# Performance work log

Hardware: AMD Instinct MI355X
Metric: run time of the kernel (lower is better)

The kernel has to match this reference:

```python
import jax, jax.numpy as jnp
import numpy as np

N_NODES = 50000
N_EDGES = 800000
N_GRAPHS = 2048
NODE_F = 30
EDGE_F = 8
HID = 32
HEADS = 4
NEG_SLOPE = 0.2


def _gat_conv(x, src, dst, eattr, W, a_src, a_dst, We, a_edge, b):
    # x: [N, Fin]; src/dst: [E'] (self-loops already appended); eattr: [E', edge_dim]
    N = x.shape[0]
    H, C = a_src.shape
    h = (x @ W).reshape(N, H, C)                     # [N,H,C]
    e = (eattr @ We).reshape(-1, H, C)               # [E',H,C]
    al_s = jnp.sum(h * a_src, axis=-1)               # [N,H]
    al_d = jnp.sum(h * a_dst, axis=-1)               # [N,H]
    al_e = jnp.sum(e * a_edge, axis=-1)              # [E',H]
    alpha = al_s[src] + al_d[dst] + al_e             # [E',H]
    alpha = jax.nn.leaky_relu(alpha, NEG_SLOPE)
    # segment softmax over destination nodes (every node has a self-loop)
    mx = jax.ops.segment_max(alpha, dst, num_segments=N)
    alpha = jnp.exp(alpha - mx[dst])
    den = jax.ops.segment_sum(alpha, dst, num_segments=N)
    alpha = alpha / (den[dst] + 1e-16)
    msg = h[src] * alpha[:, :, None]                 # [E',H,C]
    out = jax.ops.segment_sum(msg, dst, num_segments=N)  # [N,H,C]
    return out.reshape(N, H * C) + b


def _make_params(key):
    ks = jax.random.split(key, 32)
    i = 0
    p = {}
    def nxt(shape, scale=0.1):
        nonlocal i
        k = ks[i]; i += 1
        return jax.random.normal(k, shape, dtype=jnp.float32) * scale
    dims = [(NODE_F, HEADS * HID), (HEADS * HID, HEADS * HID), (HEADS * HID, HEADS * HID)]
    for li, (fin, fout) in enumerate(dims, 1):
        p[f"W{li}"] = nxt((fin, fout))
        p[f"att_src{li}"] = nxt((HEADS, HID))
        p[f"att_dst{li}"] = nxt((HEADS, HID))
        p[f"We{li}"] = nxt((EDGE_F, HEADS * HID))
        p[f"att_e{li}"] = nxt((HEADS, HID))
        p[f"b{li}"] = nxt((HEADS * HID,))
    p["lw1"] = nxt((HEADS * HID, HID)); p["lb1"] = nxt((HID,))
    p["lw2"] = nxt((HID, HID)); p["lb2"] = nxt((HID,))
    p["lw3"] = nxt((HID, 1)); p["lb3"] = nxt((1,))
    return p


def setup_inputs() -> dict:
    key = jax.random.key(0)
    k1, k2, k3, k4, k5 = jax.random.split(key, 5)
    x = jax.random.normal(k1, (N_NODES, NODE_F), dtype=jnp.float32)
    edge_index = jax.random.randint(k2, (2, N_EDGES), 0, N_NODES, dtype=jnp.int64)
    edge_features = jax.random.normal(k3, (N_EDGES, EDGE_F), dtype=jnp.float32)
    batch = jnp.sort(jax.random.randint(k4, (N_NODES,), 0, N_GRAPHS, dtype=jnp.int64))
    inp = {"x": x, "edge_index": edge_index, "edge_features": edge_features, "batch": batch}
    inp.update(_make_params(k5))
    return inp


def reference(x, edge_index, edge_features, batch,
              W1, att_src1, att_dst1, We1, att_e1, b1,
              W2, att_src2, att_dst2, We2, att_e2, b2,
              W3, att_src3, att_dst3, We3, att_e3, b3,
              lw1, lb1, lw2, lb2, lw3, lb3):
    N = x.shape[0]
    # add self-loops (PyG GATConv default); self-loop edge_attr = mean of edge_attr
    loop = jnp.arange(N, dtype=edge_index.dtype)
    src = jnp.concatenate([edge_index[0], loop])
    dst = jnp.concatenate([edge_index[1], loop])
    mean_e = jnp.mean(edge_features, axis=0, keepdims=True)
    eattr = jnp.concatenate([edge_features, jnp.broadcast_to(mean_e, (N, EDGE_F))], axis=0)

    h = jax.nn.relu(_gat_conv(x, src, dst, eattr, W1, att_src1, att_dst1, We1, att_e1, b1))
    h = jax.nn.relu(_gat_conv(h, src, dst, eattr, W2, att_src2, att_dst2, We2, att_e2, b2))
    h = jax.nn.relu(_gat_conv(h, src, dst, eattr, W3, att_src3, att_dst3, We3, att_e3, b3))
    # global_add_pool
    g = jax.ops.segment_sum(h, batch, num_segments=N_GRAPHS)   # [G, H*C]
    g = jax.nn.relu(g @ lw1 + lb1)
    g = jax.nn.relu(g @ lw2 + lb2)
    g = jax.nn.relu(g @ lw3 + lb3)                              # [G, 1]
    return g
```

## Files before the change

kernel.cpp:

```cpp
#include <hip/hip_runtime.h>

#define NND 50000
#define NE  800000
#define NET 850000
#define NG  2048
#define KT  32
#define SCB 196
#define MB  1024

__device__ __forceinline__ float frelu(float v){ return v > 0.f ? v : 0.f; }

__device__ __forceinline__ unsigned short f2bf(float f){
    unsigned int u = __float_as_uint(f);
    u += 0x7FFFu + ((u >> 16) & 1u);
    return (unsigned short)(u >> 16);
}

__global__ __launch_bounds__(256) void k_mean(const float4* __restrict__ ef4,
                                              float* __restrict__ partial){
    __shared__ float4 red[256];
    int t = threadIdx.x;
    int i0 = blockIdx.x * 256 + t;
    const int S = MB * 256;
    float4 a = make_float4(0.f, 0.f, 0.f, 0.f);
    for (int j = i0; j < NE * 2; j += S){
        float4 v = ef4[j];
        a.x += v.x; a.y += v.y; a.z += v.z; a.w += v.w;
    }
    red[t] = a;
    __syncthreads();
    for (int off = 128; off >= 2; off >>= 1){
        if (t < off){
            float4 o = red[t + off];
            float4 m = red[t];
            m.x += o.x; m.y += o.y; m.z += o.z; m.w += o.w;
            red[t] = m;
        }
        __syncthreads();
    }
    if (t < 8){
        float v = (t < 4) ? ((const float*)&red[0])[t]
                          : ((const float*)&red[1])[t - 4];
        partial[blockIdx.x * 8 + t] = v;
    }
}

__global__ void k_prep(const float* __restrict__ partial,
                       const float* __restrict__ We1, const float* __restrict__ ae1,
                       const float* __restrict__ We2, const float* __restrict__ ae2,
                       const float* __restrict__ We3, const float* __restrict__ ae3,
                       float* __restrict__ M, float* __restrict__ sc){
    __shared__ float me[8];
    __shared__ float pm[16][8];
    __shared__ float Ms[96];
    int t = threadIdx.x;
    {
        int ch = t & 7, seg = t >> 3;
        float s = 0.f;
        for (int j = seg; j < MB; j += 16) s += partial[j * 8 + ch];
        pm[seg][ch] = s;
    }
    __syncthreads();
    if (t < 8){
        float s = 0.f;
        for (int i = 0; i < 16; i++) s += pm[i][t];
        me[t] = s * (1.0f / NE);
    }
    if (t < 96){
        int l = t >> 5, f = (t >> 2) & 7, h = t & 3;
        const float* We = (l == 0) ? We1 : ((l == 1) ? We2 : We3);
        const float* ae = (l == 0) ? ae1 : ((l == 1) ? ae2 : ae3);
        float s = 0.f;
        for (int c = 0; c < 32; c++) s += We[f * 128 + h * 32 + c] * ae[h * 32 + c];
        M[t] = s; Ms[t] = s;
    }
    __syncthreads();
    if (t < 12){
        int l = t >> 2, h = t & 3;
        float s = 0.f;
        for (int f = 0; f < 8; f++) s += me[f] * Ms[l * 32 + f * 4 + h];
        sc[t] = s;
    }
}

__global__ __launch_bounds__(256) void k_gemm(
        const float* __restrict__ x, const float* __restrict__ W,
        const float* __restrict__ asrc, const float* __restrict__ adst,
        unsigned short* __restrict__ h, float* __restrict__ als,
        float* __restrict__ ald, int Fin){
    __shared__ float Ws[KT * 128];
    __shared__ float xst[KT * 36];
    int t  = threadIdx.x;
    int cg = t & 31;
    int rg = t >> 5;
    int r0 = blockIdx.x * 32;
    float acc[4][4] = {{0.f}};
    int nch = (Fin + KT - 1) / KT;
    for (int ch = 0; ch < nch; ch++){
        int k0 = ch * KT;
        {
            const float4* Wv = (const float4*)(W + k0 * 128);
            float4* Wsv = (float4*)Ws;
            int lim = (Fin - k0 >= KT ? KT : Fin - k0) * 32;
            for (int i = t; i < KT * 32; i += 256)
                Wsv[i] = (i < lim) ? Wv[i] : make_float4(0.f, 0.f, 0.f, 0.f);
        }
        for (int i = t; i < 32 * KT; i += 256){
            int r = i >> 5, kk = i & 31;
            int gr = r0 + r;
            float v = 0.f;
            if (gr < NND && (k0 + kk) < Fin) v = x[gr * Fin + k0 + kk];
            xst[kk * 36 + r] = v;
        }
        __syncthreads();
        #pragma unroll 8
        for (int k = 0; k < KT; k++){
            float4 xv = *(const float4*)&xst[k * 36 + rg * 4];
            float4 wv = *(const float4*)&Ws[k * 128 + cg * 4];
            acc[0][0] += xv.x * wv.x; acc[0][1] += xv.x * wv.y;
            acc[0][2] += xv.x * wv.z; acc[0][3] += xv.x * wv.w;
            acc[1][0] += xv.y * wv.x; acc[1][1] += xv.y * wv.y;
            acc[1][2] += xv.y * wv.z; acc[1][3] += xv.y * wv.w;
            acc[2][0] += xv.z * wv.x; acc[2][1] += xv.z * wv.y;
            acc[2][2] += xv.z * wv.z; acc[2][3] += xv.z * wv.w;
            acc[3][0] += xv.w * wv.x; acc[3][1] += xv.w * wv.y;
            acc[3][2] += xv.w * wv.z; acc[3][3] += xv.w * wv.w;
        }
        __syncthreads();
    }
    float4 av = *(const float4*)&asrc[cg * 4];
    float4 dv = *(const float4*)&adst[cg * 4];
    int head = cg >> 3;
    bool leader = ((cg & 7) == 0);
    #pragma unroll
    for (int r = 0; r < 4; r++){
        int gr = r0 + rg * 4 + r;
        float4 o = make_float4(acc[r][0], acc[r][1], acc[r][2], acc[r][3]);
        if (gr < NND){
            ushort4 p;
            p.x = f2bf(o.x); p.y = f2bf(o.y); p.z = f2bf(o.z); p.w = f2bf(o.w);
            *(ushort4*)&h[gr * 128 + cg * 4] = p;
        }
        float sv = o.x * av.x + o.y * av.y + o.z * av.z + o.w * av.w;
        float sd = o.x * dv.x + o.y * dv.y + o.z * dv.z + o.w * dv.w;
        sv += __shfl_down(sv, 4, 64); sd += __shfl_down(sd, 4, 64);
        sv += __shfl_down(sv, 2, 64); sd += __shfl_down(sd, 2, 64);
        sv += __shfl_down(sv, 1, 64); sd += __shfl_down(sd, 1, 64);
        if (leader && gr < NND){
            als[gr * 4 + head] = sv;
            ald[gr * 4 + head] = sd;
        }
    }
}

__global__ void k_hist(const int* __restrict__ ei, int* __restrict__ cnt,
                       int* __restrict__ pose){
    int e = blockIdx.x * 256 + threadIdx.x;
    if (e >= NE) return;
    int d = ei[NE + e];
    pose[e] = atomicAdd(&cnt[d], 1);
}

__global__ __launch_bounds__(256) void k_scan1(const int* __restrict__ cnt,
                                               int* __restrict__ bsum){
    __shared__ int red[256];
    int t = threadIdx.x;
    int idx = blockIdx.x * 256 + t;
    red[t] = (idx < NND) ? (cnt[idx] + 1) : 0;
    __syncthreads();
    for (int off = 128; off > 0; off >>= 1){
        if (t < off) red[t] += red[t + off];
        __syncthreads();
    }
    if (t == 0) bsum[blockIdx.x] = red[0];
}

__global__ __launch_bounds__(256) void k_scan2(const int* __restrict__ bsum,
                                               int* __restrict__ boff,
                                               int* __restrict__ rs){
    __shared__ int ls[256];
    int t = threadIdx.x;
    int v = (t < SCB) ? bsum[t] : 0;
    ls[t] = v;
    __syncthreads();
    for (int off = 1; off < 256; off <<= 1){
        int u = (t >= off) ? ls[t - off] : 0;
        __syncthreads();
        ls[t] += u;
        __syncthreads();
    }
    if (t < SCB) boff[t] = ls[t] - bsum[t];
    if (t == 0)  rs[NND] = ls[255];
}

__global__ __launch_bounds__(256) void k_scan3(const int* __restrict__ cnt,
                                               const int* __restrict__ boff,
                                               int* __restrict__ rs){
    __shared__ int ls[256];
    int t = threadIdx.x;
    int idx = blockIdx.x * 256 + t;
    int v = (idx < NND) ? (cnt[idx] + 1) : 0;
    ls[t] = v;
    __syncthreads();
    for (int off = 1; off < 256; off <<= 1){
        int u = (t >= off) ? ls[t - off] : 0;
        __syncthreads();
        ls[t] += u;
        __syncthreads();
    }
    if (idx < NND) rs[idx] = boff[blockIdx.x] + ls[t] - v;
}

__global__ void k_scatter(const int* __restrict__ ei, const int* __restrict__ rs,
                          const int* __restrict__ pose, int* __restrict__ srcarr,
                          int* __restrict__ slotof){
    int e = blockIdx.x * 256 + threadIdx.x;
    if (e >= NET) return;
    if (e < NE){
        int s = ei[e], d = ei[NE + e];
        int slot = rs[d] + 1 + pose[e];
        srcarr[slot] = s;
        slotof[e] = slot;
    } else {
        int n = e - NE;
        srcarr[rs[n]] = n;
    }
}

__global__ __launch_bounds__(256) void k_weight(
        const int* __restrict__ ei, const float* __restrict__ ef,
        const float4* __restrict__ als4, const float4* __restrict__ ald4,
        const float* __restrict__ Mg, const float* __restrict__ sc4g,
        const int* __restrict__ rs, const int* __restrict__ slotof,
        float4* __restrict__ wS){
    __shared__ float Ms[32];
    __shared__ float Scs[4];
    int t = threadIdx.x;
    if (t < 32) Ms[t] = Mg[t];
    if (t < 4)  Scs[t] = sc4g[t];
    __syncthreads();
    int e = blockIdx.x * 256 + t;
    if (e < NE){
        int s = ei[e], d = ei[NE + e];
        const float4* efp = (const float4*)ef;
        float4 u = efp[e * 2], v = efp[e * 2 + 1];
        float4 A = als4[s], D = ald4[d];
        float4 w;
        float* wp = &w.x;
        const float* Ap = &A.x; const float* Dp = &D.x;
        #pragma unroll
        for (int h = 0; h < 4; h++){
            float ae = u.x * Ms[0 + h]  + u.y * Ms[4 + h]
                     + u.z * Ms[8 + h]  + u.w * Ms[12 + h]
                     + v.x * Ms[16 + h] + v.y * Ms[20 + h]
                     + v.z * Ms[24 + h] + v.w * Ms[28 + h];
            float a = Ap[h] + Dp[h] + ae;
            a = a > 0.f ? a : 0.2f * a;
            wp[h] = __expf(a);
        }
        wS[slotof[e]] = w;
    } else if (e < NE + NND){
        int n = e - NE;
        float4 A = als4[n], D = ald4[n];
        float4 w;
        float* wp = &w.x;
        const float* Ap = &A.x; const float* Dp = &D.x;
        #pragma unroll
        for (int h = 0; h < 4; h++){
            float a = Ap[h] + Dp[h] + Scs[h];
            a = a > 0.f ? a : 0.2f * a;
            wp[h] = __expf(a);
        }
        wS[rs[n]] = w;
    }
}

__global__ __launch_bounds__(256) void k_gather(
        const int* __restrict__ srcarr, const int* __restrict__ rs,
        const float* __restrict__ wS,
        const unsigned int* __restrict__ HU,
        const float* __restrict__ b, float* __restrict__ out){
    int wid  = threadIdx.x >> 6;
    int lane = threadIdx.x & 63;
    int n = blockIdx.x * 4 + wid;
    int start = rs[n], end = rs[n + 1];
    int cnt = end - start;
    int mh = lane >> 4;
    float ax = 0.f, ay = 0.f, accw = 0.f;

    int s[8]; float w[8];
    int k = 0;
    if (cnt >= 8){
        #pragma unroll
        for (int j = 0; j < 8; j++){
            int i = start + j;
            s[j] = srcarr[i];
            w[j] = wS[i * 4 + mh];
        }
    }
    while (k + 8 <= cnt){
        int cs[8]; float cw[8];
        #pragma unroll
        for (int j = 0; j < 8; j++){ cs[j] = s[j]; cw[j] = w[j]; }
        k += 8;
        if (k + 8 <= cnt){
            #pragma unroll
            for (int j = 0; j < 8; j++){
                int i = start + k + j;
                s[j] = srcarr[i];
                w[j] = wS[i * 4 + mh];
            }
        }
        unsigned int hv[8];
        #pragma unroll
        for (int j = 0; j < 8; j++) hv[j] = HU[cs[j] * 64 + lane];
        #pragma unroll
        for (int j = 0; j < 8; j++){
            float lo = __uint_as_float(hv[j] << 16);
            float hi = __uint_as_float(hv[j] & 0xFFFF0000u);
            ax += cw[j] * lo;
            ay += cw[j] * hi;
            accw += cw[j];
        }
    }
    int rem = cnt - k;
    if (rem > 0){
        int ts[8]; float tw[8];
        #pragma unroll
        for (int j = 0; j < 8; j++){
            bool v = j < rem;
            int i = v ? (start + k + j) : start;
            ts[j] = srcarr[i];
            tw[j] = v ? wS[i * 4 + mh] : 0.f;
        }
        unsigned int hv[8];
        #pragma unroll
        for (int j = 0; j < 8; j++) hv[j] = HU[ts[j] * 64 + lane];
        #pragma unroll
        for (int j = 0; j < 8; j++){
            float lo = __uint_as_float(hv[j] << 16);
            float hi = __uint_as_float(hv[j] & 0xFFFF0000u);
            ax += tw[j] * lo;
            ay += tw[j] * hi;
            accw += tw[j];
        }
    }
    float inv = 1.f / (accw + 1e-16f);
    int c0 = 2 * lane;
    float2 o;
    o.x = frelu(ax * inv + b[c0]);
    o.y = frelu(ay * inv + b[c0 + 1]);
    ((float2*)out)[n * 64 + lane] = o;
}

__global__ __launch_bounds__(128) void k_pool(const float* __restrict__ y,
                                              const int* __restrict__ batch,
                                              float* __restrict__ g){
    int c = threadIdx.x;
    int n0 = blockIdx.x * 32;
    if (n0 >= NND) return;
    int cur = batch[n0];
    float s = 0.f;
    for (int k = 0; k < 32; k++){
        int n = n0 + k;
        if (n >= NND) break;
        int bg = batch[n];
        if (bg != cur){
            atomicAdd(&g[cur * 128 + c], s);
            s = 0.f; cur = bg;
        }
        s += y[n * 128 + c];
    }
    atomicAdd(&g[cur * 128 + c], s);
}

__global__ void k_mlp(const float* __restrict__ g,
                      const float* __restrict__ lw1, const float* __restrict__ lb1,
                      const float* __restrict__ lw2, const float* __restrict__ lb2,
                      const float* __restrict__ lw3, const float* __restrict__ lb3,
                      float* __restrict__ out){
    __shared__ float t1[4][32];
    __shared__ float t2[4][32];
    int tid = threadIdx.x, sub = tid >> 5, j = tid & 31;
    int gi = blockIdx.x * 4 + sub;
    const float* gr = g + gi * 128;
    float s = lb1[j];
    for (int c = 0; c < 128; c++) s += gr[c] * lw1[c * 32 + j];
    t1[sub][j] = frelu(s);
    __syncthreads();
    float s2 = lb2[j];
    for (int k = 0; k < 32; k++) s2 += t1[sub][k] * lw2[k * 32 + j];
    t2[sub][j] = frelu(s2);
    __syncthreads();
    if (j == 0){
        float o = lb3[0];
        for (int k = 0; k < 32; k++) o += t2[sub][k] * lw3[k];
        out[gi] = frelu(o);
    }
}

extern "C" void kernel_launch(void* const* d_in, const int* in_sizes, int n_in,
                              void* d_out, int out_size, void* d_ws, size_t ws_size,
                              hipStream_t stream) {
    const float* x     = (const float*)d_in[0];
    const int*   ei    = (const int*)  d_in[1];
    const float* ef    = (const float*)d_in[2];
    const int*   batch = (const int*)  d_in[3];
    const float* W[3]   = {(const float*)d_in[4],  (const float*)d_in[10], (const float*)d_in[16]};
    const float* as_[3] = {(const float*)d_in[5],  (const float*)d_in[11], (const float*)d_in[17]};
    const float* ad_[3] = {(const float*)d_in[6],  (const float*)d_in[12], (const float*)d_in[18]};
    const float* We[3]  = {(const float*)d_in[7],  (const float*)d_in[13], (const float*)d_in[19]};
    const float* ae[3]  = {(const float*)d_in[8],  (const float*)d_in[14], (const float*)d_in[20]};
    const float* b_[3]  = {(const float*)d_in[9],  (const float*)d_in[15], (const float*)d_in[21]};
    const float* lw1 = (const float*)d_in[22]; const float* lb1 = (const float*)d_in[23];
    const float* lw2 = (const float*)d_in[24]; const float* lb2 = (const float*)d_in[25];
    const float* lw3 = (const float*)d_in[26]; const float* lb3 = (const float*)d_in[27];

    float* ws = (float*)d_ws;
    float* Bx   = ws;
    float* Hbf  = Bx + 6400000;
    float* wSf  = Hbf + 6400000;
    float* als  = wSf + 3400000;
    float* ald  = als + 200000;
    float* g    = ald + 200000;
    float* partial = g + 262144;
    float* M    = partial + MB * 8;
    float* sc   = M + 96;
    int*   srcarr = (int*)(sc + 16);
    int*   slotof = srcarr + NET;
    int*   pose   = slotof + NE;
    int*   rs     = pose + NE;
    int*   cnt    = rs + NND + 4;
    int*   bsum   = cnt + NND;
    int*   boff   = bsum + SCB;

    unsigned short* Hb = (unsigned short*)Hbf;

    hipMemsetAsync(cnt, 0, NND * sizeof(int), stream);
    hipMemsetAsync(g,   0, NG * 128 * sizeof(float), stream);

    k_mean<<<MB, 256, 0, stream>>>((const float4*)ef, partial);
    k_prep<<<1, 128, 0, stream>>>(partial, We[0], ae[0], We[1], ae[1], We[2], ae[2], M, sc);

    k_hist<<<(NE + 255) / 256, 256, 0, stream>>>(ei, cnt, pose);
    k_scan1<<<SCB, 256, 0, stream>>>(cnt, bsum);
    k_scan2<<<1, 256, 0, stream>>>(bsum, boff, rs);
    k_scan3<<<SCB, 256, 0, stream>>>(cnt, boff, rs);
    k_scatter<<<(NET + 255) / 256, 256, 0, stream>>>(ei, rs, pose, srcarr, slotof);

    const float* xin = x;
    for (int l = 0; l < 3; l++){
        int Fin = (l == 0) ? 30 : 128;
        k_gemm<<<(NND + 31) / 32, 256, 0, stream>>>(xin, W[l], as_[l], ad_[l],
                                                    Hb, als, ald, Fin);
        k_weight<<<(NE + NND + 255) / 256, 256, 0, stream>>>(
            ei, ef, (const float4*)als, (const float4*)ald,
            M + l * 32, sc + l * 4, rs, slotof, (float4*)wSf);
        k_gather<<<NND / 4, 256, 0, stream>>>(srcarr, rs, wSf,
                                              (const unsigned int*)Hb, b_[l], Bx);
        xin = Bx;
    }

    k_pool<<<(NND + 31) / 32, 128, 0, stream>>>(Bx, batch, g);
    k_mlp<<<NG / 4, 128, 0, stream>>>(g, lw1, lb1, lw2, lb2, lw3, lb3, (float*)d_out);
}
```

Before: 475.2 us.

## Rewrite node GEMM with bf16 MFMA and LDS-staged epilogue

Replaces the FP32 scalar register-tiled node-feature GEMM with a bf16 MFMA (16x16x32) kernel that processes 64 rows per block. The input is converted to bf16 in LDS, and the per-head attention dot products are computed from the bf16 results staged in LDS. Output rows are then written with coalesced 16-byte stores. The feature width is made a template parameter. Inputs are now rounded to bf16 before the multiply, which lowers precision, and attention logits are computed from rounded h instead of the fp32 accumulators.

Measured after the change: 472.6 us. No clear change (-0.5%).

```diff
diff --git a/kernel.cpp b/kernel.cpp
--- a/kernel.cpp
+++ b/kernel.cpp
@@ -4,9 +4,11 @@
 #define NE  800000
 #define NET 850000
 #define NG  2048
-#define KT  32
 #define SCB 196
 #define MB  1024
+
+typedef __attribute__((ext_vector_type(8))) short short8;
+typedef __attribute__((ext_vector_type(4))) float float4v;
 
 __device__ __forceinline__ float frelu(float v){ return v > 0.f ? v : 0.f; }
 
@@ -83,73 +85,87 @@
     }
 }
 
+template<int FIN, int FINR>
 __global__ __launch_bounds__(256) void k_gemm(
         const float* __restrict__ x, const float* __restrict__ W,
         const float* __restrict__ asrc, const float* __restrict__ adst,
         unsigned short* __restrict__ h, float* __restrict__ als,
-        float* __restrict__ ald, int Fin){
-    __shared__ float Ws[KT * 128];
-    __shared__ float xst[KT * 36];
-    int t  = threadIdx.x;
-    int cg = t & 31;
-    int rg = t >> 5;
-    int r0 = blockIdx.x * 32;
-    float acc[4][4] = {{0.f}};
-    int nch = (Fin + KT - 1) / KT;
-    for (int ch = 0; ch < nch; ch++){
-        int k0 = ch * KT;
-        {
-            const float4* Wv = (const float4*)(W + k0 * 128);
-            float4* Wsv = (float4*)Ws;
-            int lim = (Fin - k0 >= KT ? KT : Fin - k0) * 32;
-            for (int i = t; i < KT * 32; i += 256)
-                Wsv[i] = (i < lim) ? Wv[i] : make_float4(0.f, 0.f, 0.f, 0.f);
-        }
-        for (int i = t; i < 32 * KT; i += 256){
-            int r = i >> 5, kk = i & 31;
-            int gr = r0 + r;
-            float v = 0.f;
-            if (gr < NND && (k0 + kk) < Fin) v = x[gr * Fin + k0 + kk];
-            xst[kk * 36 + r] = v;
-        }
-        __syncthreads();
-        #pragma unroll 8
-        for (int k = 0; k < KT; k++){
-            float4 xv = *(const float4*)&xst[k * 36 + rg * 4];
-            float4 wv = *(const float4*)&Ws[k * 128 + cg * 4];
-            acc[0][0] += xv.x * wv.x; acc[0][1] += xv.x * wv.y;
-            acc[0][2] += xv.x * wv.z; acc[0][3] += xv.x * wv.w;
-            acc[1][0] += xv.y * wv.x; acc[1][1] += xv.y * wv.y;
-            acc[1][2] += xv.y * wv.z; acc[1][3] += xv.y * wv.w;
-            acc[2][0] += xv.z * wv.x; acc[2][1] += xv.z * wv.y;
-            acc[2][2] += xv.z * wv.z; acc[2][3] += xv.z * wv.w;
-            acc[3][0] += xv.w * wv.x; acc[3][1] += xv.w * wv.y;
-            acc[3][2] += xv.w * wv.z; acc[3][3] += xv.w * wv.w;
-        }
-        __syncthreads();
-    }
-    float4 av = *(const float4*)&asrc[cg * 4];
-    float4 dv = *(const float4*)&adst[cg * 4];
-    int head = cg >> 3;
-    bool leader = ((cg & 7) == 0);
+        float* __restrict__ ald){
+    constexpr int KS = FIN + 8;
+    constexpr int SZ1 = 64 * KS + 128 * KS;
+    constexpr int SZ2 = 64 * 136;
+    constexpr int LSZ = SZ1 > SZ2 ? SZ1 : SZ2;
+    __shared__ unsigned short lds[LSZ];
+    unsigned short* xa = lds;
+    unsigned short* wb = lds + 64 * KS;
+    int t = threadIdx.x;
+    int r0 = blockIdx.x * 64;
+
+    for (int i = t; i < 64 * (FIN / 2); i += 256){
+        int r = i / (FIN / 2), kp = i % (FIN / 2);
+        int gr = r0 + r, k = 2 * kp;
+        float v0 = 0.f, v1 = 0.f;
+        if (gr < NND){
+            if (k     < FINR) v0 = x[gr * FINR + k];
+            if (k + 1 < FINR) v1 = x[gr * FINR + k + 1];
+        }
+        unsigned int pk = (unsigned int)f2bf(v0) | ((unsigned int)f2bf(v1) << 16);
+        *(unsigned int*)&xa[r * KS + k] = pk;
+    }
+    for (int i = t; i < 128 * (FIN / 2); i += 256){
+        int n = i & 127, kp = i >> 7, k = 2 * kp;
+        float v0 = (k     < FINR) ? W[k * 128 + n]       : 0.f;
+        float v1 = (k + 1 < FINR) ? W[(k + 1) * 128 + n] : 0.f;
+        unsigned int pk = (unsigned int)f2bf(v0) | ((unsigned int)f2bf(v1) << 16);
+        *(unsigned int*)&wb[n * KS + k] = pk;
+    }
+    __syncthreads();
+
+    int wv = t >> 6, lane = t & 63;
+    int quad = lane >> 4, lrow = lane & 15;
+    int arow = wv * 16 + lrow;
+    int koff = quad * 8;
+    float4v acc[8];
     #pragma unroll
-    for (int r = 0; r < 4; r++){
-        int gr = r0 + rg * 4 + r;
-        float4 o = make_float4(acc[r][0], acc[r][1], acc[r][2], acc[r][3]);
-        if (gr < NND){
-            ushort4 p;
-            p.x = f2bf(o.x); p.y = f2bf(o.y); p.z = f2bf(o.z); p.w = f2bf(o.w);
-            *(ushort4*)&h[gr * 128 + cg * 4] = p;
-        }
-        float sv = o.x * av.x + o.y * av.y + o.z * av.z + o.w * av.w;
-        float sd = o.x * dv.x + o.y * dv.y + o.z * dv.z + o.w * dv.w;
-        sv += __shfl_down(sv, 4, 64); sd += __shfl_down(sd, 4, 64);
-        sv += __shfl_down(sv, 2, 64); sd += __shfl_down(sd, 2, 64);
-        sv += __shfl_down(sv, 1, 64); sd += __shfl_down(sd, 1, 64);
-        if (leader && gr < NND){
-            als[gr * 4 + head] = sv;
-            ald[gr * 4 + head] = sd;
-        }
+    for (int nt = 0; nt < 8; nt++) acc[nt] = (float4v){0.f, 0.f, 0.f, 0.f};
+    #pragma unroll
+    for (int ks = 0; ks < FIN / 32; ks++){
+        short8 af = *(const short8*)&xa[arow * KS + ks * 32 + koff];
+        #pragma unroll
+        for (int nt = 0; nt < 8; nt++){
+            short8 bf = *(const short8*)&wb[(nt * 16 + lrow) * KS + ks * 32 + koff];
+            acc[nt] = __builtin_amdgcn_mfma_f32_16x16x32_bf16(af, bf, acc[nt], 0, 0, 0);
+        }
+    }
+    __syncthreads();
+    unsigned short* hb = lds;
+    #pragma unroll
+    for (int nt = 0; nt < 8; nt++){
+        #pragma unroll
+        for (int reg = 0; reg < 4; reg++){
+            int lr = wv * 16 + quad * 4 + reg;
+            hb[lr * 136 + nt * 16 + lrow] = f2bf(acc[nt][reg]);
+        }
+    }
+    __syncthreads();
+    {
+        int r = t >> 2, hd = t & 3;
+        int gr = r0 + r;
+        float sa = 0.f, sd = 0.f;
+        const unsigned short* hp = &hb[r * 136 + hd * 32];
+        #pragma unroll
+        for (int c = 0; c < 32; c++){
+            float hv = __uint_as_float(((unsigned int)hp[c]) << 16);
+            sa += hv * asrc[hd * 32 + c];
+            sd += hv * adst[hd * 32 + c];
+        }
+        if (gr < NND){ als[gr * 4 + hd] = sa; ald[gr * 4 + hd] = sd; }
+    }
+    for (int i = t; i < 64 * 16; i += 256){
+        int r = i >> 4, c8 = i & 15;
+        int gr = r0 + r;
+        if (gr < NND)
+            *(int4*)&h[gr * 128 + c8 * 8] = *(const int4*)&hb[r * 136 + c8 * 8];
     }
 }
 
@@ -448,11 +464,15 @@
     k_scan3<<<SCB, 256, 0, stream>>>(cnt, boff, rs);
     k_scatter<<<(NET + 255) / 256, 256, 0, stream>>>(ei, rs, pose, srcarr, slotof);
 
+    const int GB = (NND + 63) / 64;
     const float* xin = x;
     for (int l = 0; l < 3; l++){
-        int Fin = (l == 0) ? 30 : 128;
-        k_gemm<<<(NND + 31) / 32, 256, 0, stream>>>(xin, W[l], as_[l], ad_[l],
-                                                    Hb, als, ald, Fin);
+        if (l == 0)
+            k_gemm<32, 30><<<GB, 256, 0, stream>>>(xin, W[l], as_[l], ad_[l],
+                                                   Hb, als, ald);
+        else
+            k_gemm<128, 128><<<GB, 256, 0, stream>>>(xin, W[l], as_[l], ad_[l],
+                                                     Hb, als, ald);
         k_weight<<<(NE + NND + 255) / 256, 256, 0, stream>>>(
             ei, ef, (const float4*)als, (const float4*)ald,
             M + l * 32, sc + l * 4, rs, slotof, (float4*)wSf);
```
